# Kernel tuning notes

Measured on AMD Instinct MI355X. Metric: run time of the kernel, lower is better.

## Reference

```python
import jax, jax.numpy as jnp
import numpy as np

K = 3  # kernel size (3x3 deformable unfold, dilation 1, padding 1, stride 1)


def _bilinear_sample_max(xb, off):
    """xb: [C,H,W] feature map; off: [18,H,W] offsets (dy,dx per tap).
    Returns per-channel max over the 9 bilinearly sampled taps: [C,H,W].
    Out-of-bounds samples use zero padding (deform-conv convention)."""
    C, H, W = xb.shape
    # base sampling grid: (h + kh - 1 + dy, w + kw - 1 + dx)
    kh, kw = jnp.meshgrid(jnp.arange(K) - 1, jnp.arange(K) - 1, indexing="ij")
    kh = kh.reshape(K * K).astype(xb.dtype)          # [9]
    kw = kw.reshape(K * K).astype(xb.dtype)          # [9]
    hh = jnp.arange(H, dtype=xb.dtype)
    ww = jnp.arange(W, dtype=xb.dtype)
    off = off.reshape(K * K, 2, H, W)                 # [9,2,H,W], (dy,dx)
    py = hh[None, :, None] + kh[:, None, None] + off[:, 0]   # [9,H,W]
    px = ww[None, None, :] + kw[:, None, None] + off[:, 1]   # [9,H,W]

    y0 = jnp.floor(py)
    x0 = jnp.floor(px)
    wy = py - y0                                      # [9,H,W]
    wx = px - x0
    y0i = y0.astype(jnp.int32)
    x0i = x0.astype(jnp.int32)

    def gather(yi, xi):
        valid = (yi >= 0) & (yi < H) & (xi >= 0) & (xi < W)   # [9,H,W]
        yc = jnp.clip(yi, 0, H - 1)
        xc = jnp.clip(xi, 0, W - 1)
        v = xb[:, yc, xc]                             # [C,9,H,W]
        return v * valid[None].astype(xb.dtype)

    v00 = gather(y0i, x0i)
    v01 = gather(y0i, x0i + 1)
    v10 = gather(y0i + 1, x0i)
    v11 = gather(y0i + 1, x0i + 1)
    # bilinear blend -> [C,9,H,W]
    samp = (v00 * ((1 - wy) * (1 - wx))[None]
            + v01 * ((1 - wy) * wx)[None]
            + v10 * (wy * (1 - wx))[None]
            + v11 * (wy * wx)[None])
    return samp.max(axis=1)                           # [C,H,W]


def setup_inputs() -> dict:
    key = jax.random.key(0)
    k1, k2, k3 = jax.random.split(key, 3)
    B, C, H, W = 4, 256, 100, 100
    x = jax.random.normal(k1, (B, C, H, W), dtype=jnp.float32)
    offset = jax.random.normal(k2, (B, 2 * K * K, H, W), dtype=jnp.float32)
    # conv0: nn.Conv2d(C, 1, 1) with normal_init std=0.01, bias 0
    w0 = jax.random.normal(k3, (1, C), dtype=jnp.float32) * 0.01
    b0 = jnp.zeros((1,), dtype=jnp.float32)
    return {"x": x, "offset": offset, "w0": w0, "b0": b0}


def reference(x, offset, w0, b0):
    # deformable 3x3 unfold + per-channel max over taps  -> [B,C,H,W]
    feat = jax.vmap(_bilinear_sample_max)(x, offset)
    # 1x1 conv (C -> 1) + sigmoid                        -> [B,1,H,W]
    out = jnp.einsum("bchw,oc->bohw", feat, w0) + b0[None, :, None, None]
    return jax.nn.sigmoid(out)
```

## Files before the change

### kernel.cpp

```cpp
#include <hip/hip_runtime.h>
#include <hip/hip_fp16.h>
#include <math.h>

#define BB 4
#define CC 256
#define HH 100
#define WW 100
#define HWP (HH * WW)
#define NPIX (BB * HWP)

#define CGN 4
#define CHB 64
#define ROWB (CHB * 2)

#define XT_BYTES ((size_t)NPIX * CC * 2)
#define FEAT_BYTES ((size_t)CGN * NPIX * 4)

#define NT_BLOCKS (BB * HH)

#define TILE 8
#define HALO 16
#define TPD 13
#define TPI (TPD * TPD)
#define NBLK (BB * CGN * TPI)

#define KGSPLIT 6

static __device__ inline uint pk_max_f16(uint a, uint b) {
    uint r;
    asm("v_pk_max_f16 %0, %1, %2" : "=v"(r) : "v"(a), "v"(b));
    return r;
}

__global__ __launch_bounds__(256) void prep_kernel(
    const float* __restrict__ x, ushort* __restrict__ xT) {
    __shared__ uint tileT[WW][CC / 2 + 1];
    int bh = blockIdx.x;
    int b = bh / HH;
    int h = bh - b * HH;
    const float* src = x + (size_t)b * CC * HWP + (size_t)h * WW;

    for (int idx = threadIdx.x; idx < (CC / 2) * 25; idx += 256) {
        int c2 = idx / 25;
        int w4 = idx - c2 * 25;
        const float* p0 = src + (size_t)(2 * c2) * HWP + w4 * 4;
        float4 va = *reinterpret_cast<const float4*>(p0);
        float4 vb = *reinterpret_cast<const float4*>(p0 + HWP);
        __half2 h0 = __floats2half2_rn(va.x, vb.x);
        __half2 h1 = __floats2half2_rn(va.y, vb.y);
        __half2 h2 = __floats2half2_rn(va.z, vb.z);
        __half2 h3 = __floats2half2_rn(va.w, vb.w);
        tileT[w4 * 4 + 0][c2] = *reinterpret_cast<uint*>(&h0);
        tileT[w4 * 4 + 1][c2] = *reinterpret_cast<uint*>(&h1);
        tileT[w4 * 4 + 2][c2] = *reinterpret_cast<uint*>(&h2);
        tileT[w4 * 4 + 3][c2] = *reinterpret_cast<uint*>(&h3);
    }
    __syncthreads();

    uint2* dstu = reinterpret_cast<uint2*>(xT);
    for (int idx = threadIdx.x; idx < WW * (CC / 4); idx += 256) {
        int w = idx >> 6;
        int c4 = idx & 63;
        int cg = c4 >> 4;
        size_t o = ((size_t)((b * CGN + cg) * HH + h) * WW + w) * 16 + (c4 & 15);
        dstu[o] = make_uint2(tileT[w][2 * c4], tileT[w][2 * c4 + 1]);
    }
}

__global__ __launch_bounds__(512, 6) void deform_tiled5_kernel(
    const char* __restrict__ xTg, const float* __restrict__ off,
    const float* __restrict__ w0, float* __restrict__ feat) {
    __shared__ uint4 halo4[HALO * HALO * 8];
    __shared__ int4 geomL[TILE * TILE * 9];

    int lb = (blockIdx.x & 7) * (NBLK / 8) + (blockIdx.x >> 3);
    int pl = lb / TPI;
    int tile = lb - pl * TPI;
    int b = pl >> 2, cg = pl & 3;
    int tyi = tile / TPD;
    int ty = tyi * TILE;
    int tx = (tile - tyi * TPD) * TILE;
    int sy = min(max(ty - 4, 0), HH - HALO);
    int sx = min(max(tx - 4, 0), WW - HALO);
    int plane = (b * CGN + cg) * HH;

    const char* hbase = xTg + ((size_t)(plane + sy) * WW + sx) * ROWB;
#pragma unroll
    for (int it = 0; it < 4; ++it) {
        int i = it * 512 + threadIdx.x;
        int strip = i >> 7;
        int within = i & 127;
        uint4 v = *reinterpret_cast<const uint4*>(
            hbase + (size_t)strip * (WW * ROWB) + ((size_t)within << 4));
        int pos = (strip << 4) + (within >> 3);
        int c = within & 7;
        halo4[(pos << 3) + (c ^ (pos & 7))] = v;
    }
    {
        const float* offb = off + (size_t)b * 18 * HWP;
        for (int i = threadIdx.x; i < 9 * 64; i += 512) {
            int k = i >> 6;
            int px = i & 63;
            int r = px >> 3, c = px & 7;
            int h2 = min(ty + r, HH - 1);
            int w2 = min(tx + c, WW - 1);
            int hw = h2 * WW + w2;
            float dy = offb[(size_t)(2 * k) * HWP + hw];
            float dx = offb[(size_t)(2 * k + 1) * HWP + hw];
            int kh = k / 3 - 1;
            int kw = k - (k / 3) * 3 - 1;
            float py = (float)(h2 + kh) + dy;
            float px_ = (float)(w2 + kw) + dx;
            float y0f = floorf(py), x0f = floorf(px_);
            float wy = py - y0f, wx = px_ - x0f;
            int y0 = (int)y0f, x0 = (int)x0f;
            int y1 = y0 + 1, x1 = x0 + 1;
            bool vy0 = (y0 >= 0) && (y0 < HH);
            bool vy1 = (y1 >= 0) && (y1 < HH);
            bool vx0 = (x0 >= 0) && (x0 < WW);
            bool vx1 = (x1 >= 0) && (x1 < WW);
            int yc0 = min(max(y0, 0), HH - 1);
            int yc1 = min(max(y1, 0), HH - 1);
            int xc0 = min(max(x0, 0), WW - 1);
            int xc1 = min(max(x1, 0), WW - 1);
            float w00 = (1.f - wy) * (1.f - wx) * (float)(vy0 && vx0);
            float w01 = (1.f - wy) * wx * (float)(vy0 && vx1);
            float w10 = wy * (1.f - wx) * (float)(vy1 && vx0);
            float w11 = wy * wx * (float)(vy1 && vx1);
            int packed = yc0 | (yc1 << 8) | (xc0 << 16) | (xc1 << 24);
            __half2 hw01 = __floats2half2_rn(w00, w01);
            __half2 hw23 = __floats2half2_rn(w10, w11);
            geomL[px * 9 + k] =
                make_int4(packed, *reinterpret_cast<int*>(&hw01),
                          *reinterpret_cast<int*>(&hw23), 0);
        }
    }
    __syncthreads();

    int lane = threadIdx.x & 63;
    int wid = threadIdx.x >> 6;
    int sub = lane >> 3;
    int cl = lane & 7;
    int h = ty + wid, wc = tx + sub;
    bool pvalid = (h < HH) && (wc < WW);
    int pi = wid * 8 + sub;
    int lo = cl << 4;

    uint m0 = 0xFC00FC00u, m1 = m0, m2 = m0, m3 = m0;

#pragma unroll
    for (int k = 0; k < 9; ++k) {
        int4 rec = geomL[pi * 9 + k];
        int packed = rec.x;
        int yc0 = packed & 255, yc1 = (packed >> 8) & 255;
        int xc0 = (packed >> 16) & 255, xc1 = (int)((uint)packed >> 24);
        uint4 u00, u01, u10, u11;
        bool useLds = false;
        if (k < KGSPLIT) {
            int ry0 = yc0 - sy, ry1 = yc1 - sy;
            int cx0 = xc0 - sx, cx1 = xc1 - sx;
            bool inh = ((uint)ry0 < (uint)HALO) & ((uint)ry1 < (uint)HALO) &
                       ((uint)cx0 < (uint)HALO) & ((uint)cx1 < (uint)HALO);
            useLds = __all(inh);
            if (useLds) {
                int p00 = (ry0 << 4) + cx0, p01 = (ry0 << 4) + cx1;
                int p10 = (ry1 << 4) + cx0, p11 = (ry1 << 4) + cx1;
                u00 = halo4[(p00 << 3) + (cl ^ (cx0 & 7))];
                u01 = halo4[(p01 << 3) + (cl ^ (cx1 & 7))];
                u10 = halo4[(p10 << 3) + (cl ^ (cx0 & 7))];
                u11 = halo4[(p11 << 3) + (cl ^ (cx1 & 7))];
            }
        }
        if (!useLds) {
            u00 = *reinterpret_cast<const uint4*>(
                xTg + ((size_t)(plane + yc0) * WW + xc0) * ROWB + lo);
            u01 = *reinterpret_cast<const uint4*>(
                xTg + ((size_t)(plane + yc0) * WW + xc1) * ROWB + lo);
            u10 = *reinterpret_cast<const uint4*>(
                xTg + ((size_t)(plane + yc1) * WW + xc0) * ROWB + lo);
            u11 = *reinterpret_cast<const uint4*>(
                xTg + ((size_t)(plane + yc1) * WW + xc1) * ROWB + lo);
        }

        uint uwa = (uint)rec.y, uwb = (uint)rec.z;
        uint w00u = (uwa & 0xffffu) | (uwa << 16);
        uint w01u = (uwa >> 16) | (uwa & 0xffff0000u);
        uint w10u = (uwb & 0xffffu) | (uwb << 16);
        uint w11u = (uwb >> 16) | (uwb & 0xffff0000u);
        __half2 w00 = *reinterpret_cast<__half2*>(&w00u);
        __half2 w01 = *reinterpret_cast<__half2*>(&w01u);
        __half2 w10 = *reinterpret_cast<__half2*>(&w10u);
        __half2 w11 = *reinterpret_cast<__half2*>(&w11u);

        __half2 a; uint au;
#define BLEND(out, f)                                                     \
        au = u00.f; a = *reinterpret_cast<__half2*>(&au);                 \
        { __half2 acc = __hmul2(a, w00);                                  \
          au = u01.f; a = *reinterpret_cast<__half2*>(&au);               \
          acc = __hfma2(a, w01, acc);                                     \
          au = u10.f; a = *reinterpret_cast<__half2*>(&au);               \
          acc = __hfma2(a, w10, acc);                                     \
          au = u11.f; a = *reinterpret_cast<__half2*>(&au);               \
          acc = __hfma2(a, w11, acc);                                     \
          out = pk_max_f16(out, *reinterpret_cast<uint*>(&acc)); }
        BLEND(m0, x)
        BLEND(m1, y)
        BLEND(m2, z)
        BLEND(m3, w)
#undef BLEND
    }

    const float4* wv = reinterpret_cast<const float4*>(w0) + (cg * 16 + cl * 2);
    float4 wq0 = wv[0], wq1 = wv[1];
    float2 f0 = __half22float2(*reinterpret_cast<__half2*>(&m0));
    float2 f1 = __half22float2(*reinterpret_cast<__half2*>(&m1));
    float2 f2 = __half22float2(*reinterpret_cast<__half2*>(&m2));
    float2 f3 = __half22float2(*reinterpret_cast<__half2*>(&m3));
    float part = f0.x * wq0.x + f0.y * wq0.y + f1.x * wq0.z + f1.y * wq0.w +
                 f2.x * wq1.x + f2.y * wq1.y + f3.x * wq1.z + f3.y * wq1.w;
#pragma unroll
    for (int d = 4; d > 0; d >>= 1) part += __shfl_down(part, d, 8);
    if (cl == 0 && pvalid)
        feat[(size_t)cg * NPIX + b * HWP + h * WW + wc] = part;
}

__global__ __launch_bounds__(256) void combine_kernel(
    const float* __restrict__ feat, const float* __restrict__ b0,
    float* __restrict__ out) {
    int i = blockIdx.x * 256 + threadIdx.x;
    if (i < NPIX) {
        float z = feat[i] + feat[NPIX + i] + feat[2 * NPIX + i] +
                  feat[3 * NPIX + i] + b0[0];
        out[i] = 1.f / (1.f + expf(-z));
    }
}

__global__ __launch_bounds__(128) void deform_fallback_kernel(
    const float* __restrict__ x, const float* __restrict__ off,
    const float* __restrict__ w0, const float* __restrict__ b0,
    float* __restrict__ out) {
    int p = blockIdx.x;
    int b = p / HWP;
    int hw = p - b * HWP;
    int h = hw / WW;
    int w = hw - h * WW;
    int tid = threadIdx.x;

    const float* offp = off + (size_t)b * 18 * HWP + hw;
    const float* xb = x + (size_t)b * CC * HWP + (size_t)(2 * tid) * HWP;

    float m0 = -INFINITY, m1 = -INFINITY;

#pragma unroll
    for (int k = 0; k < 9; ++k) {
        int kh = k / 3 - 1;
        int kw = k - (k / 3) * 3 - 1;
        float dy = offp[(size_t)(2 * k) * HWP];
        float dx = offp[(size_t)(2 * k + 1) * HWP];
        float py = (float)(h + kh) + dy;
        float px = (float)(w + kw) + dx;
        float y0f = floorf(py), x0f = floorf(px);
        float wy = py - y0f, wx = px - x0f;
        int y0 = (int)y0f, x0 = (int)x0f;
        int y1 = y0 + 1, x1 = x0 + 1;
        bool vy0 = (y0 >= 0) && (y0 < HH);
        bool vy1 = (y1 >= 0) && (y1 < HH);
        bool vx0 = (x0 >= 0) && (x0 < WW);
        bool vx1 = (x1 >= 0) && (x1 < WW);
        int yc0 = min(max(y0, 0), HH - 1);
        int yc1 = min(max(y1, 0), HH - 1);
        int xc0 = min(max(x0, 0), WW - 1);
        int xc1 = min(max(x1, 0), WW - 1);
        float w00 = (1.f - wy) * (1.f - wx) * (float)(vy0 && vx0);
        float w01 = (1.f - wy) * wx * (float)(vy0 && vx1);
        float w10 = wy * (1.f - wx) * (float)(vy1 && vx0);
        float w11 = wy * wx * (float)(vy1 && vx1);

        int o00 = yc0 * WW + xc0, o01 = yc0 * WW + xc1;
        int o10 = yc1 * WW + xc0, o11 = yc1 * WW + xc1;
        float s0 = xb[o00] * w00 + xb[o01] * w01 + xb[o10] * w10 + xb[o11] * w11;
        float s1 = xb[o00 + HWP] * w00 + xb[o01 + HWP] * w01 +
                   xb[o10 + HWP] * w10 + xb[o11 + HWP] * w11;
        m0 = fmaxf(m0, s0);
        m1 = fmaxf(m1, s1);
    }

    float2 wv = reinterpret_cast<const float2*>(w0)[tid];
    float partial = m0 * wv.x + m1 * wv.y;
#pragma unroll
    for (int d = 32; d > 0; d >>= 1) partial += __shfl_down(partial, d, 64);

    __shared__ float red[2];
    if ((tid & 63) == 0) red[tid >> 6] = partial;
    __syncthreads();
    if (tid == 0) {
        float z = red[0] + red[1] + b0[0];
        out[p] = 1.f / (1.f + expf(-z));
    }
}

extern "C" void kernel_launch(void* const* d_in, const int* in_sizes, int n_in,
                              void* d_out, int out_size, void* d_ws, size_t ws_size,
                              hipStream_t stream) {
    const float* x   = (const float*)d_in[0];
    const float* off = (const float*)d_in[1];
    const float* w0  = (const float*)d_in[2];
    const float* b0  = (const float*)d_in[3];
    float* out = (float*)d_out;

    if (ws_size >= XT_BYTES + FEAT_BYTES) {
        char* xT = (char*)d_ws;
        float* feat = (float*)((char*)d_ws + XT_BYTES);
        prep_kernel<<<NT_BLOCKS, 256, 0, stream>>>(x, (ushort*)xT);
        deform_tiled5_kernel<<<NBLK, 512, 0, stream>>>(xT, off, w0, feat);
        combine_kernel<<<(NPIX + 255) / 256, 256, 0, stream>>>(feat, b0, out);
    } else {
        deform_fallback_kernel<<<NPIX, 128, 0, stream>>>(x, off, w0, b0, out);
    }
}
```

Measured before the change: 44.78 us.

## Prefetch last two taps from global early, use op_sel packed FMAs, split prep

The deform kernel now issues the global loads for taps 7 and 8 before the LDS-backed loop over taps 0-6, so their latency overlaps the earlier work. KGSPLIT rises from 6 to 7, and the bilinear blend uses inline v_pk_fma_f16 with op_sel so the per-tap weight broadcast shuffles disappear. The prep transpose kernel is split across two channel halves, doubling the block count and halving its shared-memory tile. The prefetched taps hold 8 extra uint4 registers per thread, which may cost occupancy.

```diff
diff --git a/kernel.cpp b/kernel.cpp
--- a/kernel.cpp
+++ b/kernel.cpp
@@ -16,7 +16,7 @@
 #define XT_BYTES ((size_t)NPIX * CC * 2)
 #define FEAT_BYTES ((size_t)CGN * NPIX * 4)
 
-#define NT_BLOCKS (BB * HH)
+#define NP_BLOCKS (BB * HH * 2)
 
 #define TILE 8
 #define HALO 16
@@ -24,23 +24,44 @@
 #define TPI (TPD * TPD)
 #define NBLK (BB * CGN * TPI)
 
-#define KGSPLIT 6
+#define KGSPLIT 7
 
 static __device__ inline uint pk_max_f16(uint a, uint b) {
     uint r;
     asm("v_pk_max_f16 %0, %1, %2" : "=v"(r) : "v"(a), "v"(b));
     return r;
 }
+static __device__ inline uint pk_mul_bl(uint a, uint w) {
+    uint r;
+    asm("v_pk_mul_f16 %0, %1, %2 op_sel:[0,0] op_sel_hi:[1,0]"
+        : "=v"(r) : "v"(a), "v"(w));
+    return r;
+}
+static __device__ inline uint pk_fma_bl(uint a, uint w, uint c) {
+    uint r;
+    asm("v_pk_fma_f16 %0, %1, %2, %3 op_sel:[0,0,0] op_sel_hi:[1,0,1]"
+        : "=v"(r) : "v"(a), "v"(w), "v"(c));
+    return r;
+}
+static __device__ inline uint pk_fma_bh(uint a, uint w, uint c) {
+    uint r;
+    asm("v_pk_fma_f16 %0, %1, %2, %3 op_sel:[0,1,0] op_sel_hi:[1,1,1]"
+        : "=v"(r) : "v"(a), "v"(w), "v"(c));
+    return r;
+}
 
 __global__ __launch_bounds__(256) void prep_kernel(
     const float* __restrict__ x, ushort* __restrict__ xT) {
-    __shared__ uint tileT[WW][CC / 2 + 1];
-    int bh = blockIdx.x;
-    int b = bh / HH;
-    int h = bh - b * HH;
-    const float* src = x + (size_t)b * CC * HWP + (size_t)h * WW;
-
-    for (int idx = threadIdx.x; idx < (CC / 2) * 25; idx += 256) {
+    __shared__ uint tileT[WW][65];
+    int bid = blockIdx.x;
+    int b = bid / (HH * 2);
+    int rem = bid - b * (HH * 2);
+    int h = rem >> 1;
+    int half = rem & 1;
+    const float* src = x + (size_t)b * CC * HWP + (size_t)(half * 128) * HWP +
+                       (size_t)h * WW;
+
+    for (int idx = threadIdx.x; idx < 64 * 25; idx += 256) {
         int c2 = idx / 25;
         int w4 = idx - c2 * 25;
         const float* p0 = src + (size_t)(2 * c2) * HWP + w4 * 4;
@@ -58,16 +79,17 @@
     __syncthreads();
 
     uint2* dstu = reinterpret_cast<uint2*>(xT);
-    for (int idx = threadIdx.x; idx < WW * (CC / 4); idx += 256) {
-        int w = idx >> 6;
-        int c4 = idx & 63;
-        int cg = c4 >> 4;
-        size_t o = ((size_t)((b * CGN + cg) * HH + h) * WW + w) * 16 + (c4 & 15);
-        dstu[o] = make_uint2(tileT[w][2 * c4], tileT[w][2 * c4 + 1]);
-    }
-}
-
-__global__ __launch_bounds__(512, 6) void deform_tiled5_kernel(
+    for (int idx = threadIdx.x; idx < WW * 32; idx += 256) {
+        int w = idx >> 5;
+        int s = idx & 31;
+        int cg = half * 2 + (s >> 4);
+        int c4in = s & 15;
+        size_t o = ((size_t)((b * CGN + cg) * HH + h) * WW + w) * 16 + c4in;
+        dstu[o] = make_uint2(tileT[w][2 * s], tileT[w][2 * s + 1]);
+    }
+}
+
+__global__ __launch_bounds__(512, 6) void deform_tiled6_kernel(
     const char* __restrict__ xTg, const float* __restrict__ off,
     const float* __restrict__ w0, float* __restrict__ feat) {
     __shared__ uint4 halo4[HALO * HALO * 8];
@@ -148,30 +170,63 @@
 
     uint m0 = 0xFC00FC00u, m1 = m0, m2 = m0, m3 = m0;
 
-#pragma unroll
-    for (int k = 0; k < 9; ++k) {
+    int4 rec7 = geomL[pi * 9 + 7];
+    int4 rec8 = geomL[pi * 9 + 8];
+    uint4 g7[4], g8[4];
+#define GLOAD(dst, rec)                                                      \
+    {                                                                        \
+        int pk_ = rec.x;                                                     \
+        int yc0_ = pk_ & 255, yc1_ = (pk_ >> 8) & 255;                       \
+        int xc0_ = (pk_ >> 16) & 255, xc1_ = (int)((uint)pk_ >> 24);         \
+        dst[0] = *reinterpret_cast<const uint4*>(                            \
+            xTg + ((size_t)(plane + yc0_) * WW + xc0_) * ROWB + lo);         \
+        dst[1] = *reinterpret_cast<const uint4*>(                            \
+            xTg + ((size_t)(plane + yc0_) * WW + xc1_) * ROWB + lo);         \
+        dst[2] = *reinterpret_cast<const uint4*>(                            \
+            xTg + ((size_t)(plane + yc1_) * WW + xc0_) * ROWB + lo);         \
+        dst[3] = *reinterpret_cast<const uint4*>(                            \
+            xTg + ((size_t)(plane + yc1_) * WW + xc1_) * ROWB + lo);         \
+    }
+    GLOAD(g7, rec7)
+    GLOAD(g8, rec8)
+#undef GLOAD
+
+#define BLEND4(u00, u01, u10, u11, wa, wb)                                   \
+    {                                                                        \
+        uint acc;                                                            \
+        acc = pk_mul_bl(u00.x, wa); acc = pk_fma_bh(u01.x, wa, acc);         \
+        acc = pk_fma_bl(u10.x, wb, acc); acc = pk_fma_bh(u11.x, wb, acc);    \
+        m0 = pk_max_f16(m0, acc);                                            \
+        acc = pk_mul_bl(u00.y, wa); acc = pk_fma_bh(u01.y, wa, acc);         \
+        acc = pk_fma_bl(u10.y, wb, acc); acc = pk_fma_bh(u11.y, wb, acc);    \
+        m1 = pk_max_f16(m1, acc);                                            \
+        acc = pk_mul_bl(u00.z, wa); acc = pk_fma_bh(u01.z, wa, acc);         \
+        acc = pk_fma_bl(u10.z, wb, acc); acc = pk_fma_bh(u11.z, wb, acc);    \
+        m2 = pk_max_f16(m2, acc);                                            \
+        acc = pk_mul_bl(u00.w, wa); acc = pk_fma_bh(u01.w, wa, acc);         \
+        acc = pk_fma_bl(u10.w, wb, acc); acc = pk_fma_bh(u11.w, wb, acc);    \
+        m3 = pk_max_f16(m3, acc);                                            \
+    }
+
+#pragma unroll
+    for (int k = 0; k < KGSPLIT; ++k) {
         int4 rec = geomL[pi * 9 + k];
         int packed = rec.x;
         int yc0 = packed & 255, yc1 = (packed >> 8) & 255;
         int xc0 = (packed >> 16) & 255, xc1 = (int)((uint)packed >> 24);
+        int ry0 = yc0 - sy, ry1 = yc1 - sy;
+        int cx0 = xc0 - sx, cx1 = xc1 - sx;
+        bool inh = ((uint)ry0 < (uint)HALO) & ((uint)ry1 < (uint)HALO) &
+                   ((uint)cx0 < (uint)HALO) & ((uint)cx1 < (uint)HALO);
         uint4 u00, u01, u10, u11;
-        bool useLds = false;
-        if (k < KGSPLIT) {
-            int ry0 = yc0 - sy, ry1 = yc1 - sy;
-            int cx0 = xc0 - sx, cx1 = xc1 - sx;
-            bool inh = ((uint)ry0 < (uint)HALO) & ((uint)ry1 < (uint)HALO) &
-                       ((uint)cx0 < (uint)HALO) & ((uint)cx1 < (uint)HALO);
-            useLds = __all(inh);
-            if (useLds) {
-                int p00 = (ry0 << 4) + cx0, p01 = (ry0 << 4) + cx1;
-                int p10 = (ry1 << 4) + cx0, p11 = (ry1 << 4) + cx1;
-                u00 = halo4[(p00 << 3) + (cl ^ (cx0 & 7))];
-                u01 = halo4[(p01 << 3) + (cl ^ (cx1 & 7))];
-                u10 = halo4[(p10 << 3) + (cl ^ (cx0 & 7))];
-                u11 = halo4[(p11 << 3) + (cl ^ (cx1 & 7))];
-            }
-        }
-        if (!useLds) {
+        if (__all(inh)) {
+            int p00 = (ry0 << 4) + cx0, p01 = (ry0 << 4) + cx1;
+            int p10 = (ry1 << 4) + cx0, p11 = (ry1 << 4) + cx1;
+            u00 = halo4[(p00 << 3) + (cl ^ (cx0 & 7))];
+            u01 = halo4[(p01 << 3) + (cl ^ (cx1 & 7))];
+            u10 = halo4[(p10 << 3) + (cl ^ (cx0 & 7))];
+            u11 = halo4[(p11 << 3) + (cl ^ (cx1 & 7))];
+        } else {
             u00 = *reinterpret_cast<const uint4*>(
                 xTg + ((size_t)(plane + yc0) * WW + xc0) * ROWB + lo);
             u01 = *reinterpret_cast<const uint4*>(
@@ -181,34 +236,17 @@
             u11 = *reinterpret_cast<const uint4*>(
                 xTg + ((size_t)(plane + yc1) * WW + xc1) * ROWB + lo);
         }
-
-        uint uwa = (uint)rec.y, uwb = (uint)rec.z;
-        uint w00u = (uwa & 0xffffu) | (uwa << 16);
-        uint w01u = (uwa >> 16) | (uwa & 0xffff0000u);
-        uint w10u = (uwb & 0xffffu) | (uwb << 16);
-        uint w11u = (uwb >> 16) | (uwb & 0xffff0000u);
-        __half2 w00 = *reinterpret_cast<__half2*>(&w00u);
-        __half2 w01 = *reinterpret_cast<__half2*>(&w01u);
-        __half2 w10 = *reinterpret_cast<__half2*>(&w10u);
-        __half2 w11 = *reinterpret_cast<__half2*>(&w11u);
-
-        __half2 a; uint au;
-#define BLEND(out, f)                                                     \
-        au = u00.f; a = *reinterpret_cast<__half2*>(&au);                 \
-        { __half2 acc = __hmul2(a, w00);                                  \
-          au = u01.f; a = *reinterpret_cast<__half2*>(&au);               \
-          acc = __hfma2(a, w01, acc);                                     \
-          au = u10.f; a = *reinterpret_cast<__half2*>(&au);               \
-          acc = __hfma2(a, w10, acc);                                     \
-          au = u11.f; a = *reinterpret_cast<__half2*>(&au);               \
-          acc = __hfma2(a, w11, acc);                                     \
-          out = pk_max_f16(out, *reinterpret_cast<uint*>(&acc)); }
-        BLEND(m0, x)
-        BLEND(m1, y)
-        BLEND(m2, z)
-        BLEND(m3, w)
-#undef BLEND
-    }
+        uint wa = (uint)rec.y, wb = (uint)rec.z;
+        BLEND4(u00, u01, u10, u11, wa, wb)
+    }
+
+    {
+        uint wa = (uint)rec7.y, wb = (uint)rec7.z;
+        BLEND4(g7[0], g7[1], g7[2], g7[3], wa, wb)
+        wa = (uint)rec8.y; wb = (uint)rec8.z;
+        BLEND4(g8[0], g8[1], g8[2], g8[3], wa, wb)
+    }
+#undef BLEND4
 
     const float4* wv = reinterpret_cast<const float4*>(w0) + (cg * 16 + cl * 2);
     float4 wq0 = wv[0], wq1 = wv[1];
@@ -311,8 +349,8 @@
     if (ws_size >= XT_BYTES + FEAT_BYTES) {
         char* xT = (char*)d_ws;
         float* feat = (float*)((char*)d_ws + XT_BYTES);
-        prep_kernel<<<NT_BLOCKS, 256, 0, stream>>>(x, (ushort*)xT);
-        deform_tiled5_kernel<<<NBLK, 512, 0, stream>>>(xT, off, w0, feat);
+        prep_kernel<<<NP_BLOCKS, 256, 0, stream>>>(x, (ushort*)xT);
+        deform_tiled6_kernel<<<NBLK, 512, 0, stream>>>(xT, off, w0, feat);
         combine_kernel<<<(NPIX + 255) / 256, 256, 0, stream>>>(feat, b0, out);
     } else {
         deform_fallback_kernel<<<NPIX, 128, 0, stream>>>(x, off, w0, b0, out);
```

After: 59.69 us. 33.3% more time.
